# Kernel optimization log

Hardware: AMD Instinct MI355X
Metric: run time of the kernel (lower is better)

Reference implementation:

```python
import jax, jax.numpy as jnp
import numpy as np

WS = 7  # window_size
SHIFT = 3  # shift_size
NH = 4  # num_heads
EPS = 1e-5


def layer_norm(x, g, b):
    mu = jnp.mean(x, axis=-1, keepdims=True)
    var = jnp.mean(jnp.square(x - mu), axis=-1, keepdims=True)
    return (x - mu) * jax.lax.rsqrt(var + EPS) * g + b


def setup_inputs() -> dict:
    key = jax.random.key(0)
    ks = jax.random.split(key, 12)
    B, H, W, C = 64, 56, 56, 128
    hid = int(C * 3.0)
    s = lambda fan: 1.0 / np.sqrt(fan)
    return {
        "x": jax.random.normal(ks[0], (B, H * W, C), jnp.float32),
        "g1": jnp.ones((C,), jnp.float32),
        "be1": jnp.zeros((C,), jnp.float32),
        "Wqkv": jax.random.normal(ks[1], (3 * C, C), jnp.float32) * s(C),
        "bqkv": jnp.zeros((3 * C,), jnp.float32),
        "Wproj": jax.random.normal(ks[2], (C, C), jnp.float32) * s(C),
        "bproj": jnp.zeros((C,), jnp.float32),
        "g2": jnp.ones((C,), jnp.float32),
        "be2": jnp.zeros((C,), jnp.float32),
        "Wm1": jax.random.normal(ks[3], (hid, C), jnp.float32) * s(C),
        "bm1": jnp.zeros((hid,), jnp.float32),
        "Wm2": jax.random.normal(ks[4], (C, hid), jnp.float32) * s(hid),
        "bm2": jnp.zeros((C,), jnp.float32),
        "H": 56,
        "W": 56,
    }


def reference(x, g1, be1, Wqkv, bqkv, Wproj, bproj, g2, be2, Wm1, bm1, Wm2, bm2, H, W):
    B, L, C = x.shape
    shortcut = x
    h = layer_norm(x, g1, be1).reshape(B, H, W, C)
    if SHIFT > 0:
        h = jnp.roll(h, shift=(-SHIFT, -SHIFT), axis=(1, 2))
    pad_h = (WS - H % WS) % WS
    pad_w = (WS - W % WS) % WS
    if pad_h or pad_w:
        h = jnp.pad(h, ((0, 0), (0, pad_h), (0, pad_w), (0, 0)))
    Hp, Wp = H + pad_h, W + pad_w
    # window partition: [B*nW, WS*WS, C]
    h = h.reshape(B, Hp // WS, WS, Wp // WS, WS, C)
    h = h.transpose(0, 1, 3, 2, 4, 5).reshape(-1, WS * WS, C)
    # windowed attention (mask=None, matching original)
    Bw, N, _ = h.shape
    d = C // NH
    qkv = (h @ Wqkv.T + bqkv).reshape(Bw, N, 3, NH, d).transpose(2, 0, 3, 1, 4)
    q, k, v = qkv[0], qkv[1], qkv[2]  # [Bw, NH, N, d]
    attn = jax.nn.softmax(jnp.einsum('whnd,whmd->whnm', q, k) * (d ** -0.5), axis=-1)
    o = jnp.einsum('whnm,whmd->whnd', attn, v).transpose(0, 2, 1, 3).reshape(Bw, N, C)
    o = o @ Wproj.T + bproj
    # window reverse
    o = o.reshape(B, Hp // WS, Wp // WS, WS, WS, C)
    o = o.transpose(0, 1, 3, 2, 4, 5).reshape(B, Hp, Wp, C)
    if pad_h or pad_w:
        o = o[:, :H, :W, :]
    if SHIFT > 0:
        o = jnp.roll(o, shift=(SHIFT, SHIFT), axis=(1, 2))
    h = shortcut + o.reshape(B, H * W, C)
    # MLP with residual
    m = layer_norm(h, g2, be2)
    m = jax.nn.gelu(m @ Wm1.T + bm1, approximate=False) @ Wm2.T + bm2
    return h + m
```

## Files before the change

kernel.cpp:

```cpp
#include <hip/hip_runtime.h>
#include <hip/hip_bf16.h>
#include <cstdint>

typedef short bf16x8 __attribute__((ext_vector_type(8)));
typedef float f32x4 __attribute__((ext_vector_type(4)));

constexpr int Bn = 64, Hn = 56, Wn = 56, Cn = 128, Ln = 3136;
constexpr int NWIN = 4096;
constexpr int NTOK = 49;
constexpr int Mtot = NWIN * NTOK;
constexpr int HID = 384;
constexpr int SHIFT_ = 3;

__device__ __forceinline__ float bf2f(short s) {
  union { uint32_t u; float f; } c; c.u = ((uint32_t)(uint16_t)s) << 16; return c.f;
}
__device__ __forceinline__ short f2bf(float f) {
  union { float f; uint32_t u; } c; c.f = f;
  uint32_t r = (c.u + 0x7FFFu + ((c.u >> 16) & 1u)) >> 16;
  return (short)r;
}
__device__ __forceinline__ float wred(float v) {
  #pragma unroll
  for (int o = 32; o > 0; o >>= 1) v += __shfl_xor(v, o);
  return v;
}

__device__ __forceinline__ size_t plain_off(int m, int l15) {
  int win = m / NTOK, tok = m - win * NTOK;
  int b = win >> 6, wi = win & 63;
  int hr = (wi >> 3) * 7 + tok / 7 + SHIFT_; if (hr >= Hn) hr -= Hn;
  int wr = (wi & 7) * 7 + tok % 7 + SHIFT_;  if (wr >= Wn) wr -= Wn;
  return (size_t)(b * Ln + hr * Wn + wr) * Cn + l15;
}

__global__ void k_cvt4(const float* __restrict__ s0, const float* __restrict__ s1,
                       const float* __restrict__ s2, const float* __restrict__ s3,
                       short* __restrict__ d0, short* __restrict__ d1,
                       short* __restrict__ d2, short* __restrict__ d3) {
  int i = blockIdx.x * 256 + threadIdx.x;
  if (i < 49152) d0[i] = f2bf(s0[i]);
  else if (i < 65536) d1[i - 49152] = f2bf(s1[i - 49152]);
  else if (i < 114688) d2[i - 65536] = f2bf(s2[i - 65536]);
  else if (i < 163840) d3[i - 114688] = f2bf(s3[i - 114688]);
}

__global__ __launch_bounds__(256) void k_ln1(const float* __restrict__ x,
                                             const float* __restrict__ g,
                                             const float* __restrict__ be,
                                             short* __restrict__ out) {
  int wave = threadIdx.x >> 6, lane = threadIdx.x & 63;
  int row = blockIdx.x * 4 + wave;
  int win = row / NTOK, tok = row % NTOK;
  int b = win >> 6, wi = win & 63;
  int wh = wi >> 3, ww = wi & 7;
  int hr = wh * 7 + tok / 7;
  int wr = ww * 7 + tok % 7;
  int hs = hr + SHIFT_; if (hs >= Hn) hs -= Hn;
  int ws2 = wr + SHIFT_; if (ws2 >= Wn) ws2 -= Wn;
  const float* xr = x + (size_t)(b * Ln + hs * Wn + ws2) * Cn;
  float2 v = *(const float2*)(xr + lane * 2);
  float sum = wred(v.x + v.y);
  float sq  = wred(v.x * v.x + v.y * v.y);
  float mean = sum * (1.f / Cn);
  float var  = sq * (1.f / Cn) - mean * mean;
  float rstd = rsqrtf(var + 1e-5f);
  int c0 = lane * 2;
  short2 o;
  o.x = f2bf((v.x - mean) * rstd * g[c0]     + be[c0]);
  o.y = f2bf((v.y - mean) * rstd * g[c0 + 1] + be[c0 + 1]);
  *(short2*)(out + (size_t)row * Cn + c0) = o;
}

__global__ __launch_bounds__(512) void k_qkvg(const short* __restrict__ A,
                                              const short* __restrict__ W,
                                              const float* __restrict__ bias,
                                              short* __restrict__ outB) {
  __shared__ __attribute__((aligned(16))) short sW[64 * 128];
  const int t = threadIdx.x;
  const int wave = t >> 6, lane = t & 63;
  const int l15 = lane & 15, gq = lane >> 4;
  const int m_base = blockIdx.x * 128;
  const int wrow = wave * 16;
  const int kb = gq * 8;

  bf16x8 af[4];
  #pragma unroll
  for (int s = 0; s < 4; ++s)
    af[s] = *(const bf16x8*)(A + (size_t)(m_base + wrow + l15) * Cn + s * 32 + kb);

  short* b0[4];
  #pragma unroll
  for (int r = 0; r < 4; ++r) {
    int m = m_base + wrow + 4 * gq + r;
    int win = m / NTOK, tok = m - win * NTOK;
    b0[r] = outB + ((size_t)win * 3 * NTOK + tok) * Cn + l15;
  }

  #pragma unroll
  for (int nb = 0; nb < 6; ++nb) {
    __syncthreads();
    #pragma unroll
    for (int i = 0; i < 2; ++i) {
      int idx = i * 512 + t;
      int n = idx >> 4, gr = idx & 15;
      *(bf16x8*)(&sW[n * 128 + ((gr ^ (n & 7)) << 3)]) =
          *(const bf16x8*)(W + (size_t)(nb * 64 + n) * Cn + gr * 8);
    }
    __syncthreads();

    f32x4 acc[4];
    #pragma unroll
    for (int tt = 0; tt < 4; ++tt) acc[tt] = (f32x4){0.f, 0.f, 0.f, 0.f};
    #pragma unroll
    for (int s = 0; s < 4; ++s) {
      #pragma unroll
      for (int tt = 0; tt < 4; ++tt) {
        bf16x8 bfr = *(const bf16x8*)(&sW[(tt * 16 + l15) * 128 +
                                          (((s * 4 + gq) ^ (l15 & 7)) << 3)]);
        acc[tt] = __builtin_amdgcn_mfma_f32_16x16x32_bf16(af[s], bfr, acc[tt], 0, 0, 0);
      }
    }

    #pragma unroll
    for (int tt = 0; tt < 4; ++tt) {
      const int colc = nb * 64 + tt * 16;
      float bv = bias[colc + l15];
      #pragma unroll
      for (int r = 0; r < 4; ++r) {
        float v = acc[tt][r] + bv;
        b0[r][((colc >> 7) * NTOK * Cn) + (colc & 127)] = f2bf(v);
      }
    }
  }
}

__global__ __launch_bounds__(512) void k_mlp(const short* __restrict__ A,
                                             const short* __restrict__ W1,
                                             const float* __restrict__ b1,
                                             const short* __restrict__ W2,
                                             const float* __restrict__ b2,
                                             float* __restrict__ outF) {
  __shared__ __attribute__((aligned(16))) short sW1[64 * 128];
  __shared__ __attribute__((aligned(16))) short sW2[128 * 64];
  __shared__ __attribute__((aligned(16))) short sAct[128 * 64];
  const int t = threadIdx.x;
  const int wave = t >> 6, lane = t & 63;
  const int l15 = lane & 15, gq = lane >> 4;
  const int m_base = blockIdx.x * 128;
  const int wrow = wave * 16;
  const int kb = gq * 8;

  bf16x8 af[4];
  #pragma unroll
  for (int s = 0; s < 4; ++s)
    af[s] = *(const bf16x8*)(A + (size_t)(m_base + wrow + l15) * Cn + s * 32 + kb);

  f32x4 acc2[8];
  #pragma unroll
  for (int tt = 0; tt < 8; ++tt) acc2[tt] = (f32x4){0.f, 0.f, 0.f, 0.f};

  for (int nb = 0; nb < 6; ++nb) {
    __syncthreads();
    #pragma unroll
    for (int i = 0; i < 2; ++i) {
      int idx = i * 512 + t;
      int n = idx >> 4, gr = idx & 15;
      *(bf16x8*)(&sW1[n * 128 + ((gr ^ (n & 7)) << 3)]) =
          *(const bf16x8*)(W1 + (size_t)(nb * 64 + n) * Cn + gr * 8);
    }
    #pragma unroll
    for (int i = 0; i < 2; ++i) {
      int idx = i * 512 + t;
      int n = idx >> 3, gr = idx & 7;
      *(bf16x8*)(&sW2[n * 64 + ((gr ^ (n & 7)) << 3)]) =
          *(const bf16x8*)(W2 + (size_t)n * HID + nb * 64 + gr * 8);
    }
    __syncthreads();

    f32x4 acc1[4];
    #pragma unroll
    for (int tt = 0; tt < 4; ++tt) acc1[tt] = (f32x4){0.f, 0.f, 0.f, 0.f};
    #pragma unroll
    for (int s = 0; s < 4; ++s) {
      #pragma unroll
      for (int tt = 0; tt < 4; ++tt) {
        bf16x8 bfr = *(const bf16x8*)(&sW1[(tt * 16 + l15) * 128 +
                                           (((s * 4 + gq) ^ (l15 & 7)) << 3)]);
        acc1[tt] = __builtin_amdgcn_mfma_f32_16x16x32_bf16(af[s], bfr, acc1[tt], 0, 0, 0);
      }
    }
    #pragma unroll
    for (int tt = 0; tt < 4; ++tt) {
      float bb = b1[nb * 64 + tt * 16 + l15];
      #pragma unroll
      for (int r = 0; r < 4; ++r) {
        float v = acc1[tt][r] + bb;
        float u = v + 0.044715f * v * v * v;
        float e = __expf(1.5957691216f * u);
        float th = 1.f - 2.f / (e + 1.f);
        int arow = wrow + 4 * gq + r;
        int col = tt * 16 + l15;
        sAct[arow * 64 + (((col >> 3) ^ (arow & 7)) << 3) + (col & 7)]
            = f2bf(0.5f * v * (1.f + th));
      }
    }
    bf16x8 af2[2];
    #pragma unroll
    for (int sl = 0; sl < 2; ++sl)
      af2[sl] = *(const bf16x8*)(&sAct[(wrow + l15) * 64 +
                                       (((sl * 4 + gq) ^ (l15 & 7)) << 3)]);
    #pragma unroll
    for (int sl = 0; sl < 2; ++sl) {
      #pragma unroll
      for (int tt = 0; tt < 8; ++tt) {
        bf16x8 bfr = *(const bf16x8*)(&sW2[(tt * 16 + l15) * 64 +
                                           (((sl * 4 + gq) ^ (l15 & 7)) << 3)]);
        acc2[tt] = __builtin_amdgcn_mfma_f32_16x16x32_bf16(af2[sl], bfr, acc2[tt], 0, 0, 0);
      }
    }
  }

  float bb[8];
  #pragma unroll
  for (int tt = 0; tt < 8; ++tt) bb[tt] = b2[tt * 16 + l15];
  #pragma unroll
  for (int r = 0; r < 4; ++r) {
    int m = m_base + wrow + 4 * gq + r;
    float* p = outF + (size_t)m * Cn + l15;
    #pragma unroll
    for (int tt = 0; tt < 8; ++tt)
      p[tt * 16] = p[tt * 16] + acc2[tt][r] + bb[tt];
  }
}

__global__ __launch_bounds__(256) void k_proj(const short* __restrict__ A,
                                              const short* __restrict__ W,
                                              const float* __restrict__ bias,
                                              const float* __restrict__ x,
                                              const float* __restrict__ g2,
                                              const float* __restrict__ be2,
                                              float* __restrict__ hOut,
                                              short* __restrict__ lnOut) {
  __shared__ __attribute__((aligned(16))) short ldsW[128 * 128];
  const int t = threadIdx.x;
  const int wave = t >> 6, lane = t & 63;
  const int l15 = lane & 15, g = lane >> 4;
  const int m_base = blockIdx.x * 64 + wave * 16;
  const int kb = g * 8;

  size_t off[4];
  float xv[4][8];
  #pragma unroll
  for (int r = 0; r < 4; ++r) {
    int m = m_base + 4 * g + r;
    off[r] = plain_off(m, l15);
    #pragma unroll
    for (int c = 0; c < 8; ++c) xv[r][c] = x[off[r] + c * 16];
  }

  float bv[8], gv[8], bev[8];
  #pragma unroll
  for (int c = 0; c < 8; ++c) {
    bv[c] = bias[c * 16 + l15]; gv[c] = g2[c * 16 + l15]; bev[c] = be2[c * 16 + l15];
  }

  const int arow = m_base + l15;
  const int awin = arow / NTOK, atok = arow - awin * NTOK;
  const short* abase = A + (size_t)awin * 3 * NTOK * Cn + (size_t)atok * Cn;
  bf16x8 af[4];
  #pragma unroll
  for (int s = 0; s < 4; ++s)
    af[s] = *(const bf16x8*)(abase + s * 32 + kb);

  #pragma unroll
  for (int i = 0; i < 8; ++i) {
    int idx = i * 256 + t;
    int n = idx >> 4, gr = idx & 15;
    *(bf16x8*)(&ldsW[n * 128 + ((gr ^ (n & 7)) << 3)]) =
        *(const bf16x8*)(W + (size_t)n * Cn + gr * 8);
  }
  __syncthreads();

  f32x4 acc[8];
  #pragma unroll
  for (int tt = 0; tt < 8; ++tt) acc[tt] = (f32x4){0.f, 0.f, 0.f, 0.f};
  #pragma unroll
  for (int s = 0; s < 4; ++s) {
    #pragma unroll
    for (int tt = 0; tt < 8; ++tt) {
      int row = tt * 16 + l15;
      bf16x8 bfr = *(const bf16x8*)(&ldsW[row * 128 + (((s * 4 + g) ^ (l15 & 7)) << 3)]);
      acc[tt] = __builtin_amdgcn_mfma_f32_16x16x32_bf16(af[s], bfr, acc[tt], 0, 0, 0);
    }
  }

  #pragma unroll
  for (int r = 0; r < 4; ++r) {
    float hv[8];
    float s1 = 0.f, s2 = 0.f;
    #pragma unroll
    for (int tt = 0; tt < 8; ++tt) {
      hv[tt] = acc[tt][r] + bv[tt] + xv[r][tt];
      s1 += hv[tt];
      s2 += hv[tt] * hv[tt];
    }
    #pragma unroll
    for (int o = 8; o >= 1; o >>= 1) { s1 += __shfl_xor(s1, o); s2 += __shfl_xor(s2, o); }
    float mean = s1 * (1.f / Cn);
    float var  = s2 * (1.f / Cn) - mean * mean;
    float rstd = rsqrtf(var + 1e-5f);
    #pragma unroll
    for (int tt = 0; tt < 8; ++tt) {
      hOut[off[r] + tt * 16] = hv[tt];
      lnOut[off[r] + tt * 16] = f2bf((hv[tt] - mean) * rstd * gv[tt] + bev[tt]);
    }
  }
}

__global__ __launch_bounds__(256, 3) void k_attn(const short* __restrict__ qkv,
                                                 short* __restrict__ out) {
  __shared__ __attribute__((aligned(16))) short sVT[8192];
  __shared__ __attribute__((aligned(16))) short sP[4][4096];
  const int t = threadIdx.x;
  const int wave = t >> 6, lane = t & 63;
  const int l15 = lane & 15, g = lane >> 4;
  const int h = wave;
  const int win = blockIdx.x;
  const short* baseQ = qkv + (size_t)win * 3 * NTOK * Cn;
  const short* baseK = baseQ + NTOK * Cn;
  const short* baseV = baseK + NTOK * Cn;

  for (int i = t; i < NTOK * 16; i += 256) {
    int j = i >> 4, cb = (i & 15) * 8;
    int jj = j >> 3, u = j & 7;
    bf16x8 v = *(const bf16x8*)(baseV + (size_t)j * Cn + cb);
    #pragma unroll
    for (int uu = 0; uu < 8; ++uu) {
      int c = cb + uu;
      sVT[(c >> 4) * 1024 + (c & 15) * 64 + ((jj ^ (c & 7)) << 3) + u] = v[uu];
    }
  }
  for (int i = t; i < 128 * 15; i += 256) {
    int c = i / 15, j = 49 + i % 15;
    sVT[(c >> 4) * 1024 + (c & 15) * 64 + (((j >> 3) ^ (c & 7)) << 3) + (j & 7)] = 0;
  }

  bf16x8 aq[4], bk[4];
  #pragma unroll
  for (int mi = 0; mi < 4; ++mi)
    aq[mi] = *(const bf16x8*)(baseQ + (size_t)(mi * 16 + l15) * Cn + h * 32 + g * 8);
  #pragma unroll
  for (int ni = 0; ni < 4; ++ni)
    bk[ni] = *(const bf16x8*)(baseK + (size_t)(ni * 16 + l15) * Cn + h * 32 + g * 8);

  f32x4 s[4][4];
  #pragma unroll
  for (int mi = 0; mi < 4; ++mi)
    #pragma unroll
    for (int ni = 0; ni < 4; ++ni) {
      s[mi][ni] = (f32x4){0.f, 0.f, 0.f, 0.f};
      s[mi][ni] = __builtin_amdgcn_mfma_f32_16x16x32_bf16(aq[mi], bk[ni], s[mi][ni], 0, 0, 0);
    }

  const float SC = 0.17677669529663687f;
  #pragma unroll
  for (int mi = 0; mi < 4; ++mi) {
    #pragma unroll
    for (int r = 0; r < 4; ++r) {
      float a0 = s[mi][0][r] * SC, a1 = s[mi][1][r] * SC, a2 = s[mi][2][r] * SC;
      float a3 = (l15 == 0) ? s[mi][3][r] * SC : -1e30f;
      float m = fmaxf(fmaxf(a0, a1), fmaxf(a2, a3));
      #pragma unroll
      for (int o = 8; o >= 1; o >>= 1) m = fmaxf(m, __shfl_xor(m, o));
      float e0 = __expf(a0 - m), e1 = __expf(a1 - m), e2 = __expf(a2 - m);
      float e3 = (l15 == 0) ? __expf(a3 - m) : 0.f;
      float ss = e0 + e1 + e2 + e3;
      #pragma unroll
      for (int o = 8; o >= 1; o >>= 1) ss += __shfl_xor(ss, o);
      float inv = 1.f / ss;
      int rr = 4 * g + r;
      float ee[4] = {e0, e1, e2, e3};
      #pragma unroll
      for (int ni = 0; ni < 4; ++ni) {
        int col = 16 * ni + l15;
        sP[wave][(mi * 2 + (col >> 5)) * 512 + rr * 32 + (((col >> 3) & 3) * 8) + (col & 7)]
            = f2bf(ee[ni] * inv);
      }
    }
  }

  __syncthreads();

  f32x4 o_[4][2];
  #pragma unroll
  for (int mi = 0; mi < 4; ++mi)
    #pragma unroll
    for (int ni = 0; ni < 2; ++ni) o_[mi][ni] = (f32x4){0.f, 0.f, 0.f, 0.f};

  #pragma unroll
  for (int ks = 0; ks < 2; ++ks) {
    bf16x8 bv[2];
    #pragma unroll
    for (int ni = 0; ni < 2; ++ni)
      bv[ni] = *(const bf16x8*)(&sVT[(h * 2 + ni) * 1024 + l15 * 64 +
                                     (((ks * 4 + g) ^ (l15 & 7)) << 3)]);
    #pragma unroll
    for (int mi = 0; mi < 4; ++mi) {
      bf16x8 ap = *(const bf16x8*)(&sP[wave][(mi * 2 + ks) * 512 + l15 * 32 + g * 8]);
      #pragma unroll
      for (int ni = 0; ni < 2; ++ni)
        o_[mi][ni] = __builtin_amdgcn_mfma_f32_16x16x32_bf16(ap, bv[ni], o_[mi][ni], 0, 0, 0);
    }
  }

  #pragma unroll
  for (int mi = 0; mi < 4; ++mi) {
    #pragma unroll
    for (int r = 0; r < 4; ++r) {
      int i = 16 * mi + 4 * g + r;
      if (i < NTOK) {
        short* orow = out + ((size_t)win * 3 * NTOK + i) * Cn + h * 32;
        #pragma unroll
        for (int ni = 0; ni < 2; ++ni)
          orow[16 * ni + l15] = f2bf(o_[mi][ni][r]);
      }
    }
  }
}

extern "C" void kernel_launch(void* const* d_in, const int* in_sizes, int n_in,
                              void* d_out, int out_size, void* d_ws, size_t ws_size,
                              hipStream_t stream) {
  const float* x     = (const float*)d_in[0];
  const float* g1    = (const float*)d_in[1];
  const float* be1   = (const float*)d_in[2];
  const float* Wqkv  = (const float*)d_in[3];
  const float* bqkv  = (const float*)d_in[4];
  const float* Wproj = (const float*)d_in[5];
  const float* bproj = (const float*)d_in[6];
  const float* g2    = (const float*)d_in[7];
  const float* be2   = (const float*)d_in[8];
  const float* Wm1   = (const float*)d_in[9];
  const float* bm1   = (const float*)d_in[10];
  const float* Wm2   = (const float*)d_in[11];
  const float* bm2   = (const float*)d_in[12];
  float* out = (float*)d_out;

  char* ws = (char*)d_ws;
  size_t SA = (size_t)Mtot * Cn * 2;
  size_t SB = (size_t)Mtot * HID * 2;
  short* bufA = (short*)ws;
  short* bufB = (short*)(ws + SA);
  short* wq = (short*)(ws + SA + SB);
  short* wp = wq + 384 * 128;
  short* w1 = wp + 128 * 128;
  short* w2 = w1 + 384 * 128;

  k_cvt4<<<640, 256, 0, stream>>>(Wqkv, Wproj, Wm1, Wm2, wq, wp, w1, w2);

  k_ln1<<<Mtot / 4, 256, 0, stream>>>(x, g1, be1, bufA);
  k_qkvg<<<Mtot / 128, 512, 0, stream>>>(bufA, wq, bqkv, bufB);
  k_attn<<<NWIN, 256, 0, stream>>>(bufB, bufB);
  k_proj<<<Mtot / 64, 256, 0, stream>>>(bufB, wp, bproj, x, g2, be2, out, bufA);
  k_mlp<<<Mtot / 128, 512, 0, stream>>>(bufA, w1, bm1, w2, bm2, out);
}
```

Baseline: 360.1 us.

## Double-buffer MLP weight tiles in LDS with register prefetch

Loads of the W1/W2 slices for the next hidden chunk are issued into registers one iteration ahead and written to an alternate LDS buffer. This overlaps global weight loads with the MFMA work. It also drops one of the two per-iteration barriers. The cost is twice the LDS for the weight tiles (about 80KB per block) plus extra registers, which may reduce how many blocks fit on each CU.

```diff
diff --git a/kernel.cpp b/kernel.cpp
--- a/kernel.cpp
+++ b/kernel.cpp
@@ -141,8 +141,8 @@
                                              const short* __restrict__ W2,
                                              const float* __restrict__ b2,
                                              float* __restrict__ outF) {
-  __shared__ __attribute__((aligned(16))) short sW1[64 * 128];
-  __shared__ __attribute__((aligned(16))) short sW2[128 * 64];
+  __shared__ __attribute__((aligned(16))) short sW1[2][64 * 128];
+  __shared__ __attribute__((aligned(16))) short sW2[2][128 * 64];
   __shared__ __attribute__((aligned(16))) short sAct[128 * 64];
   const int t = threadIdx.x;
   const int wave = t >> 6, lane = t & 63;
@@ -151,6 +151,11 @@
   const int wrow = wave * 16;
   const int kb = gq * 8;
 
+  const int n1a = t >> 4,          g1a = t & 15;
+  const int n1b = (512 + t) >> 4,  g1b = t & 15;
+  const int n2a = t >> 3,          g2a = t & 7;
+  const int n2b = (512 + t) >> 3,  g2b = t & 7;
+
   bf16x8 af[4];
   #pragma unroll
   for (int s = 0; s < 4; ++s)
@@ -160,23 +165,36 @@
   #pragma unroll
   for (int tt = 0; tt < 8; ++tt) acc2[tt] = (f32x4){0.f, 0.f, 0.f, 0.f};
 
+  bf16x8 r1a, r1b, r2a, r2b;
+
+  r1a = *(const bf16x8*)(W1 + (size_t)n1a * Cn + g1a * 8);
+  r1b = *(const bf16x8*)(W1 + (size_t)n1b * Cn + g1b * 8);
+  r2a = *(const bf16x8*)(W2 + (size_t)n2a * HID + g2a * 8);
+  r2b = *(const bf16x8*)(W2 + (size_t)n2b * HID + g2b * 8);
+  *(bf16x8*)(&sW1[0][n1a * 128 + ((g1a ^ (n1a & 7)) << 3)]) = r1a;
+  *(bf16x8*)(&sW1[0][n1b * 128 + ((g1b ^ (n1b & 7)) << 3)]) = r1b;
+  *(bf16x8*)(&sW2[0][n2a * 64 + ((g2a ^ (n2a & 7)) << 3)]) = r2a;
+  *(bf16x8*)(&sW2[0][n2b * 64 + ((g2b ^ (n2b & 7)) << 3)]) = r2b;
+  r1a = *(const bf16x8*)(W1 + (size_t)(64 + n1a) * Cn + g1a * 8);
+  r1b = *(const bf16x8*)(W1 + (size_t)(64 + n1b) * Cn + g1b * 8);
+  r2a = *(const bf16x8*)(W2 + (size_t)n2a * HID + 64 + g2a * 8);
+  r2b = *(const bf16x8*)(W2 + (size_t)n2b * HID + 64 + g2b * 8);
+
   for (int nb = 0; nb < 6; ++nb) {
+    const int cur = nb & 1;
     __syncthreads();
-    #pragma unroll
-    for (int i = 0; i < 2; ++i) {
-      int idx = i * 512 + t;
-      int n = idx >> 4, gr = idx & 15;
-      *(bf16x8*)(&sW1[n * 128 + ((gr ^ (n & 7)) << 3)]) =
-          *(const bf16x8*)(W1 + (size_t)(nb * 64 + n) * Cn + gr * 8);
-    }
-    #pragma unroll
-    for (int i = 0; i < 2; ++i) {
-      int idx = i * 512 + t;
-      int n = idx >> 3, gr = idx & 7;
-      *(bf16x8*)(&sW2[n * 64 + ((gr ^ (n & 7)) << 3)]) =
-          *(const bf16x8*)(W2 + (size_t)n * HID + nb * 64 + gr * 8);
-    }
-    __syncthreads();
+    if (nb < 5) {
+      *(bf16x8*)(&sW1[cur ^ 1][n1a * 128 + ((g1a ^ (n1a & 7)) << 3)]) = r1a;
+      *(bf16x8*)(&sW1[cur ^ 1][n1b * 128 + ((g1b ^ (n1b & 7)) << 3)]) = r1b;
+      *(bf16x8*)(&sW2[cur ^ 1][n2a * 64 + ((g2a ^ (n2a & 7)) << 3)]) = r2a;
+      *(bf16x8*)(&sW2[cur ^ 1][n2b * 64 + ((g2b ^ (n2b & 7)) << 3)]) = r2b;
+      if (nb < 4) {
+        r1a = *(const bf16x8*)(W1 + (size_t)((nb + 2) * 64 + n1a) * Cn + g1a * 8);
+        r1b = *(const bf16x8*)(W1 + (size_t)((nb + 2) * 64 + n1b) * Cn + g1b * 8);
+        r2a = *(const bf16x8*)(W2 + (size_t)n2a * HID + (nb + 2) * 64 + g2a * 8);
+        r2b = *(const bf16x8*)(W2 + (size_t)n2b * HID + (nb + 2) * 64 + g2b * 8);
+      }
+    }
 
     f32x4 acc1[4];
     #pragma unroll
@@ -185,8 +203,8 @@
     for (int s = 0; s < 4; ++s) {
       #pragma unroll
       for (int tt = 0; tt < 4; ++tt) {
-        bf16x8 bfr = *(const bf16x8*)(&sW1[(tt * 16 + l15) * 128 +
-                                           (((s * 4 + gq) ^ (l15 & 7)) << 3)]);
+        bf16x8 bfr = *(const bf16x8*)(&sW1[cur][(tt * 16 + l15) * 128 +
+                                               (((s * 4 + gq) ^ (l15 & 7)) << 3)]);
         acc1[tt] = __builtin_amdgcn_mfma_f32_16x16x32_bf16(af[s], bfr, acc1[tt], 0, 0, 0);
       }
     }
@@ -214,8 +232,8 @@
     for (int sl = 0; sl < 2; ++sl) {
       #pragma unroll
       for (int tt = 0; tt < 8; ++tt) {
-        bf16x8 bfr = *(const bf16x8*)(&sW2[(tt * 16 + l15) * 64 +
-                                           (((sl * 4 + gq) ^ (l15 & 7)) << 3)]);
+        bf16x8 bfr = *(const bf16x8*)(&sW2[cur][(tt * 16 + l15) * 64 +
+                                               (((sl * 4 + gq) ^ (l15 & 7)) << 3)]);
         acc2[tt] = __builtin_amdgcn_mfma_f32_16x16x32_bf16(af2[sl], bfr, acc2[tt], 0, 0, 0);
       }
     }
```

New measurement: 372.4 us. 1.03x slower.
